# Kernel optimization log

Measured on AMD Instinct MI355X. Metric: run time of the kernel, lower is better.

## Reference

```python
import jax, jax.numpy as jnp
import numpy as np

N = 50000      # nodes
E = 800000     # random edges (self loops appended in reference)
B = 500        # graphs
H = 4          # attention heads
F = 64         # feature_dim (per-head out channels)
SLOPE = 0.2    # GATConv leaky_relu negative slope


def gat_layer(x, src, dst, W, att_s, att_d, b):
    # x: [N, Fin]; W: [Fin, H*F]; att_s/att_d: [H, F]; b: [H*F]
    h = (x @ W).reshape(N, H, F)                       # [N,H,F]
    a_s = jnp.einsum('nhf,hf->nh', h, att_s)           # [N,H]
    a_d = jnp.einsum('nhf,hf->nh', h, att_d)           # [N,H]
    e = jax.nn.leaky_relu(a_s[src] + a_d[dst], SLOPE)  # [E',H]
    emax = jax.ops.segment_max(e, dst, num_segments=N) # [N,H] (finite: self loops)
    ee = jnp.exp(e - emax[dst])
    denom = jax.ops.segment_sum(ee, dst, num_segments=N)
    alpha = ee / denom[dst]                            # [E',H]
    out = jax.ops.segment_sum(alpha[:, :, None] * h[src], dst, num_segments=N)
    return out.reshape(N, H * F) + b


def setup_inputs() -> dict:
    key = jax.random.key(0)
    ks = jax.random.split(key, 32)
    s = 0.05
    inp = {
        'node_features': jax.random.normal(ks[0], (N, 5), jnp.float32),
        'building_mask': jax.random.randint(ks[1], (N,), 0, 2),
        'batch': jnp.sort(jax.random.randint(ks[2], (N,), 0, B)),
        'edge_index': jax.random.randint(ks[3], (2, E), 0, N),
        'bbox_W': jax.random.normal(ks[4], (5, 64)) * s,
        'bbox_b': jnp.zeros((64,), jnp.float32),
        'mask_embed': jax.random.normal(ks[5], (2, 64)) * s,
        'node_W': jax.random.normal(ks[6], (128, 64)) * s,
        'node_b': jnp.zeros((64,), jnp.float32),
        'w0': jax.random.normal(ks[7], (64, 256)) * s,
        'as0': jax.random.normal(ks[8], (H, F)) * s,
        'ad0': jax.random.normal(ks[9], (H, F)) * s,
        'b0': jnp.zeros((256,), jnp.float32),
        'w1': jax.random.normal(ks[10], (256, 256)) * s,
        'as1': jax.random.normal(ks[11], (H, F)) * s,
        'ad1': jax.random.normal(ks[12], (H, F)) * s,
        'b1': jnp.zeros((256,), jnp.float32),
        'w2': jax.random.normal(ks[13], (256, 256)) * s,
        'as2': jax.random.normal(ks[14], (H, F)) * s,
        'ad2': jax.random.normal(ks[15], (H, F)) * s,
        'b2': jnp.zeros((256,), jnp.float32),
        'agg_W': jax.random.normal(ks[16], (832, 256)) * s,
        'agg_b': jnp.zeros((256,), jnp.float32),
        'mu_W': jax.random.normal(ks[17], (256, 256)) * s,
        'mu_b': jnp.zeros((256,), jnp.float32),
        'var_W': jax.random.normal(ks[18], (256, 256)) * s,
        'var_b': jnp.zeros((256,), jnp.float32),
    }
    return inp


def reference(node_features, building_mask, batch, edge_index,
              bbox_W, bbox_b, mask_embed, node_W, node_b,
              w0, as0, ad0, b0, w1, as1, ad1, b1, w2, as2, ad2, b2,
              agg_W, agg_b, mu_W, mu_b, var_W, var_b):
    # node featurization
    x = jax.nn.relu(node_features @ bbox_W + bbox_b)          # [N,64]
    m = jax.nn.relu(mask_embed[building_mask])                 # [N,64]
    n0 = jax.nn.relu(jnp.concatenate([x, m], -1) @ node_W + node_b)  # [N,64]

    # self loops (GATConv add_self_loops=True)
    loop = jnp.arange(N, dtype=edge_index.dtype)
    src = jnp.concatenate([edge_index[0], loop])
    dst = jnp.concatenate([edge_index[1], loop])

    g = jax.ops.segment_max(n0, batch, num_segments=B, indices_are_sorted=True)
    g_embed = [g]

    n_t = jax.nn.relu(gat_layer(n0, src, dst, w0, as0, ad0, b0))
    g_embed.append(jax.ops.segment_max(n_t, batch, num_segments=B, indices_are_sorted=True))

    for (W, a_s, a_d, b) in [(w1, as1, ad1, b1), (w2, as2, ad2, b2)]:
        n_t = jax.nn.relu(gat_layer(n_t, src, dst, W, a_s, a_d, b))
        g_embed.append(jax.ops.segment_max(n_t, batch, num_segments=B, indices_are_sorted=True))

    latent = jnp.concatenate(g_embed, -1) @ agg_W + agg_b      # [B,256]
    mu = latent @ mu_W + mu_b
    log_var = latent @ var_W + var_b
    return (mu, log_var)
```

## Files before the change

### kernel.cpp

```cpp
#include <hip/hip_runtime.h>

#define NN 50000
#define EE 800000
#define BB 500
#define SCB 196

typedef short v8s __attribute__((ext_vector_type(8)));
typedef float v4f __attribute__((ext_vector_type(4)));

__device__ __forceinline__ float bf2f(unsigned short u) {
    union { unsigned int i; float f; } v; v.i = ((unsigned int)u) << 16; return v.f;
}
__device__ __forceinline__ unsigned short f2bf(float f) {
    union { float f; unsigned int i; } v; v.f = f;
    unsigned int x = v.i;
    unsigned int r = (x + 0x7FFFu + ((x >> 16) & 1u)) >> 16;
    return (unsigned short)r;
}

__global__ void k_sentinel(float* out, float val) {
    int i = blockIdx.x * blockDim.x + threadIdx.x;
    if (i < BB * 512) out[i] = val;
}

__global__ void k_prep(const float* __restrict__ nf, const int* __restrict__ bmask,
                       const float* __restrict__ bboxW, const float* __restrict__ bboxb,
                       const float* __restrict__ membed, unsigned short* __restrict__ feat,
                       const float* __restrict__ a0, unsigned short* __restrict__ d0,
                       const float* __restrict__ a1, unsigned short* __restrict__ d1,
                       const float* __restrict__ a2, unsigned short* __restrict__ d2,
                       const float* __restrict__ a3, unsigned short* __restrict__ d3,
                       int* __restrict__ counts) {
    int g = blockIdx.x * blockDim.x + threadIdx.x;
    if (g < NN) counts[g] = 1;
    if (g < NN * 64) {
        int n = g >> 6, f = g & 63;
        float s = bboxb[f];
        for (int k = 0; k < 5; ++k) s += nf[n * 5 + k] * bboxW[k * 64 + f];
        s = fmaxf(s, 0.f);
        int bm = bmask[n]; if ((unsigned)bm > 1u) bm = 0;
        float mv = fmaxf(membed[bm * 64 + f], 0.f);
        feat[(size_t)n * 128 + f] = f2bf(s);
        feat[(size_t)n * 128 + 64 + f] = f2bf(mv);
        return;
    }
    g -= NN * 64;
    const float* in; unsigned short* out; int K, Nout, idx;
    if (g < 8192)        { in = a0; out = d0; K = 128; Nout = 64;  idx = g; }
    else if (g < 24576)  { in = a1; out = d1; K = 64;  Nout = 256; idx = g - 8192; }
    else if (g < 90112)  { in = a2; out = d2; K = 256; Nout = 256; idx = g - 24576; }
    else if (g < 155648) { in = a3; out = d3; K = 256; Nout = 256; idx = g - 90112; }
    else return;
    int k = idx / Nout, n = idx % Nout;
    out[n * K + k] = f2bf(in[idx]);
}

template <int KT, bool BR, bool ATT>
__global__ __launch_bounds__(256) void k_gemm(const unsigned short* __restrict__ A,
                                              const unsigned short* __restrict__ Bt,
                                              const float* __restrict__ bias,
                                              unsigned short* __restrict__ C, int M, int ldc,
                                              const float* __restrict__ atts, const float* __restrict__ attd,
                                              float* __restrict__ asA, float* __restrict__ adA) {
    constexpr int NT = KT / 64;
    constexpr int NB = (NT > 1) ? 2 : 1;
    __shared__ v8s As[NB][64 * 8];
    __shared__ v8s Bs[NB][64 * 8];
    __shared__ float ap[4][4][4][4][2];
    const int t = threadIdx.x;
    const int m0 = blockIdx.x * 64;
    const int n0 = blockIdx.y * 64;
    const int l = t & 63, w = t >> 6;
    const int q = l >> 4, r16 = l & 15;
    const int nloc = w * 16 + r16;

    const int sm = t >> 3, kcl = t & 7;
    const int swz = kcl ^ (sm & 7);
    const int arow0 = m0 + sm, arow1 = m0 + sm + 32;
    const unsigned short* Bp0 = Bt + (size_t)(n0 + sm) * KT + kcl * 8;
    const unsigned short* Bp1 = Bt + (size_t)(n0 + sm + 32) * KT + kcl * 8;
    const unsigned short* Ap0 = A + (size_t)arow0 * KT + kcl * 8;
    const unsigned short* Ap1 = A + (size_t)arow1 * KT + kcl * 8;

    v8s ra0, ra1, rb0, rb1;
    const v8s vz = (v8s){0, 0, 0, 0, 0, 0, 0, 0};
    auto loadT = [&](int kt) {
        ra0 = (arow0 < M) ? *(const v8s*)(Ap0 + kt * 64) : vz;
        ra1 = (arow1 < M) ? *(const v8s*)(Ap1 + kt * 64) : vz;
        rb0 = *(const v8s*)(Bp0 + kt * 64);
        rb1 = *(const v8s*)(Bp1 + kt * 64);
    };
    auto storeT = [&](int b) {
        As[b][sm * 8 + swz] = ra0;
        As[b][(sm + 32) * 8 + swz] = ra1;
        Bs[b][sm * 8 + swz] = rb0;
        Bs[b][(sm + 32) * 8 + swz] = rb1;
    };

    v4f acc[4];
#pragma unroll
    for (int i = 0; i < 4; ++i) acc[i] = (v4f){0.f, 0.f, 0.f, 0.f};

    loadT(0);
    storeT(0);
    __syncthreads();
#pragma unroll
    for (int kt = 0; kt < NT; ++kt) {
        const int b = kt & (NB - 1);
        if (kt + 1 < NT) loadT(kt + 1);
#pragma unroll
        for (int s = 0; s < 2; ++s) {
            int c = s * 4 + q;
            v8s bfr = Bs[b][nloc * 8 + (c ^ (nloc & 7))];
#pragma unroll
            for (int mt = 0; mt < 4; ++mt) {
                v8s afr = As[b][(mt * 16 + r16) * 8 + (c ^ (r16 & 7))];
                acc[mt] = __builtin_amdgcn_mfma_f32_16x16x32_bf16(afr, bfr, acc[mt], 0, 0, 0);
            }
        }
        if (kt + 1 < NT) storeT((kt + 1) & (NB - 1));
        __syncthreads();
    }

    const int col = n0 + nloc;
#pragma unroll
    for (int mt = 0; mt < 4; ++mt) {
#pragma unroll
        for (int r = 0; r < 4; ++r) {
            int row = m0 + mt * 16 + q * 4 + r;
            if (row < M) {
                float v = acc[mt][r];
                if (BR) v = fmaxf(v + bias[col], 0.f);
                C[(size_t)row * ldc + col] = f2bf(v);
            }
        }
    }
    if (ATT) {
        float sa = atts[blockIdx.y * 64 + nloc];
        float da = attd[blockIdx.y * 64 + nloc];
        float rs[4][4], rd[4][4];
#pragma unroll
        for (int mt = 0; mt < 4; ++mt)
#pragma unroll
            for (int r = 0; r < 4; ++r) { rs[mt][r] = acc[mt][r] * sa; rd[mt][r] = acc[mt][r] * da; }
#pragma unroll
        for (int d = 1; d < 16; d <<= 1) {
#pragma unroll
            for (int mt = 0; mt < 4; ++mt)
#pragma unroll
                for (int r = 0; r < 4; ++r) {
                    rs[mt][r] += __shfl_xor(rs[mt][r], d, 64);
                    rd[mt][r] += __shfl_xor(rd[mt][r], d, 64);
                }
        }
        if (r16 == 0) {
#pragma unroll
            for (int mt = 0; mt < 4; ++mt)
#pragma unroll
                for (int r = 0; r < 4; ++r) { ap[w][q][mt][r][0] = rs[mt][r]; ap[w][q][mt][r][1] = rd[mt][r]; }
        }
        __syncthreads();
        if (t < 128) {
            int row = t >> 1, which = t & 1;
            int qq = (row >> 2) & 3, mtt = row >> 4, rr = row & 3;
            float s = ap[0][qq][mtt][rr][which] + ap[1][qq][mtt][rr][which] +
                      ap[2][qq][mtt][rr][which] + ap[3][qq][mtt][rr][which];
            if (m0 + row < M) (which ? adA : asA)[(m0 + row) * 4 + blockIdx.y] = s;
        }
    }
}

__global__ void k_count(const int* __restrict__ dst, int* __restrict__ counts) {
    int e = blockIdx.x * blockDim.x + threadIdx.x;
    if (e < EE) {
        int d = dst[e];
        if ((unsigned)d < (unsigned)NN) atomicAdd(&counts[d], 1);
    }
}

__global__ __launch_bounds__(256) void k_scanA(const int* __restrict__ counts, int* __restrict__ bsum) {
    __shared__ int red[256];
    const int b = blockIdx.x, t = threadIdx.x;
    int i = b * 256 + t;
    red[t] = (i < NN) ? counts[i] : 0;
    __syncthreads();
    for (int d = 128; d > 0; d >>= 1) {
        if (t < d) red[t] += red[t + d];
        __syncthreads();
    }
    if (t == 0) bsum[b] = red[0];
}

__global__ __launch_bounds__(256) void k_scanB(const int* __restrict__ bsum, int* __restrict__ boff) {
    __shared__ int s[256];
    const int t = threadIdx.x;
    int v = (t < SCB) ? bsum[t] : 0;
    s[t] = v;
    __syncthreads();
    for (int d = 1; d < 256; d <<= 1) {
        int x = (t >= d) ? s[t - d] : 0;
        __syncthreads();
        s[t] += x;
        __syncthreads();
    }
    if (t < SCB) boff[t] = s[t] - v;
}

__global__ __launch_bounds__(256) void k_scanC(const int* __restrict__ counts, const int* __restrict__ boff,
                                               int* __restrict__ off, int* __restrict__ cur) {
    __shared__ int s[256];
    const int b = blockIdx.x, t = threadIdx.x;
    int i = b * 256 + t;
    int v = (i < NN) ? counts[i] : 0;
    s[t] = v;
    __syncthreads();
    for (int d = 1; d < 256; d <<= 1) {
        int x = (t >= d) ? s[t - d] : 0;
        __syncthreads();
        s[t] += x;
        __syncthreads();
    }
    int excl = s[t] - v + boff[b];
    if (i < NN) { off[i] = excl; cur[i] = excl; }
    if (i == NN - 1) off[NN] = excl + v;
}

#define SCAT_K 256
__global__ __launch_bounds__(256) void k_scatter(const int* __restrict__ ei, int* __restrict__ cur,
                                                 int* __restrict__ csr) {
    const int p = blockIdx.x & 7;
    const int j = blockIdx.x >> 3;
    const int plo = p * (NN / 8), phi = plo + (NN / 8);
    const int TOT = EE + NN;
    const int chunk = (TOT + SCAT_K - 1) / SCAT_K;
    const int e1 = min((j + 1) * chunk, TOT);
    for (int e = j * chunk + (int)threadIdx.x; e < e1; e += 256) {
        int d = (e < EE) ? ei[EE + e] : (e - EE);
        if (d < plo || d >= phi) continue;
        int s = (e < EE) ? ei[e] : d;
        if ((unsigned)s >= (unsigned)NN) s = d;
        int pos = atomicAdd(&cur[d], 1);
        csr[pos] = s;
    }
}

__global__ __launch_bounds__(256) void k_agg(const unsigned short* __restrict__ h,
                                             const float* __restrict__ asA, const float* __restrict__ adA,
                                             const int* __restrict__ off, const int* __restrict__ csr,
                                             const float* __restrict__ bias,
                                             unsigned short* __restrict__ nout, int base) {
    __shared__ int   sL[4][64];
    __shared__ float wL[4][64][4];
    const int nd4 = threadIdx.x >> 6;
    const int node = base + blockIdx.x * 4 + nd4;
    const int l = threadIdx.x & 63;
    const int hl = l >> 4, k16 = l & 15;
    const int o0 = off[node];
    const int deg = off[node + 1] - o0;
    const int dcap = deg < 64 ? deg : 64;
    const float ad4 = adA[node * 4 + hl];
    float sm = 0.f;
    for (int k = k16; k < dcap; k += 16) {
        int s = csr[o0 + k];
        if (hl == 0) sL[nd4][k] = s;
        float e = asA[s * 4 + hl] + ad4;
        e = e > 0.f ? e : 0.2f * e;
        float w = __expf(e);
        wL[nd4][k][hl] = w;
        sm += w;
    }
    for (int k = 64 + k16; k < deg; k += 16) {
        int s = csr[o0 + k];
        float e = asA[s * 4 + hl] + ad4;
        e = e > 0.f ? e : 0.2f * e;
        sm += __expf(e);
    }
#pragma unroll
    for (int d = 1; d < 16; d <<= 1) sm += __shfl_xor(sm, d, 64);
    const float rden = 1.f / sm;
    __syncthreads();
    float a0 = 0.f, a1 = 0.f, a2 = 0.f, a3 = 0.f;
    const int c = l * 4;
    int k = 0;
    for (; k + 4 <= dcap; k += 4) {
        int s0 = sL[nd4][k], s1 = sL[nd4][k + 1], s2 = sL[nd4][k + 2], s3 = sL[nd4][k + 3];
        float w0 = wL[nd4][k][hl], w1 = wL[nd4][k + 1][hl], w2 = wL[nd4][k + 2][hl], w3 = wL[nd4][k + 3][hl];
        ushort4 h0 = *(const ushort4*)(h + (size_t)s0 * 256 + c);
        ushort4 h1 = *(const ushort4*)(h + (size_t)s1 * 256 + c);
        ushort4 h2 = *(const ushort4*)(h + (size_t)s2 * 256 + c);
        ushort4 h3 = *(const ushort4*)(h + (size_t)s3 * 256 + c);
        a0 += w0 * bf2f(h0.x) + w1 * bf2f(h1.x) + w2 * bf2f(h2.x) + w3 * bf2f(h3.x);
        a1 += w0 * bf2f(h0.y) + w1 * bf2f(h1.y) + w2 * bf2f(h2.y) + w3 * bf2f(h3.y);
        a2 += w0 * bf2f(h0.z) + w1 * bf2f(h1.z) + w2 * bf2f(h2.z) + w3 * bf2f(h3.z);
        a3 += w0 * bf2f(h0.w) + w1 * bf2f(h1.w) + w2 * bf2f(h2.w) + w3 * bf2f(h3.w);
    }
    for (; k < dcap; ++k) {
        int s = sL[nd4][k];
        float w = wL[nd4][k][hl];
        ushort4 hv = *(const ushort4*)(h + (size_t)s * 256 + c);
        a0 += w * bf2f(hv.x); a1 += w * bf2f(hv.y); a2 += w * bf2f(hv.z); a3 += w * bf2f(hv.w);
    }
    for (int k2 = 64; k2 < deg; ++k2) {
        int s = csr[o0 + k2];
        float e = asA[s * 4 + hl] + ad4;
        e = e > 0.f ? e : 0.2f * e;
        float w = __expf(e);
        ushort4 hv = *(const ushort4*)(h + (size_t)s * 256 + c);
        a0 += w * bf2f(hv.x); a1 += w * bf2f(hv.y); a2 += w * bf2f(hv.z); a3 += w * bf2f(hv.w);
    }
    float4 bv = *(const float4*)(bias + c);
    ushort4 o;
    o.x = f2bf(fmaxf(a0 * rden + bv.x, 0.f));
    o.y = f2bf(fmaxf(a1 * rden + bv.y, 0.f));
    o.z = f2bf(fmaxf(a2 * rden + bv.z, 0.f));
    o.w = f2bf(fmaxf(a3 * rden + bv.w, 0.f));
    *(ushort4*)(nout + (size_t)node * 256 + c) = o;
}

__global__ __launch_bounds__(256) void k_gmaxseg(const unsigned short* __restrict__ nt, int cols,
                                                 const int* __restrict__ batch,
                                                 float* __restrict__ gcat, int gbase) {
    __shared__ float red[256];
    const int b = blockIdx.x, t = threadIdx.x;
    const int lane = t & 63, chunk = t >> 6;
    const int c = blockIdx.y * 64 + lane;
    int lo = 0, hi = NN;
    while (lo < hi) { int mid = (lo + hi) >> 1; if (batch[mid] < b) lo = mid + 1; else hi = mid; }
    int lo2 = lo, hi2 = NN;
    while (lo2 < hi2) { int mid = (lo2 + hi2) >> 1; if (batch[mid] < b + 1) lo2 = mid + 1; else hi2 = mid; }
    float m = 0.f;
    for (int n = lo + chunk; n < lo2; n += 4)
        m = fmaxf(m, bf2f(nt[(size_t)n * cols + c]));
    red[t] = m;
    __syncthreads();
    if (chunk == 0) {
        m = fmaxf(fmaxf(m, red[64 + lane]), fmaxf(red[128 + lane], red[192 + lane]));
        gcat[b * 832 + gbase + c] = m;
    }
}

__global__ __launch_bounds__(256) void k_head1(const float* __restrict__ gcat,
                                               const float* __restrict__ aggW, const float* __restrict__ aggb,
                                               float* __restrict__ latent) {
    __shared__ float gr[832 * 4];
    __shared__ float part[4][4][64];
    const int t = threadIdx.x;
    const int g0 = blockIdx.x * 4, c0 = blockIdx.y * 64;
    for (int i = t; i < 832 * 4; i += 256) {
        int k = i >> 2, g = i & 3;
        gr[i] = gcat[(g0 + g) * 832 + k];
    }
    __syncthreads();
    const int w = t >> 6, l = t & 63;
    const float* wp = aggW + c0 + l;
    float a0 = 0.f, a1 = 0.f, a2 = 0.f, a3 = 0.f;
    const int k0 = w * 208;
#pragma unroll 4
    for (int k = k0; k < k0 + 208; ++k) {
        float wv = wp[(size_t)k * 256];
        float4 gv = *(const float4*)&gr[k * 4];
        a0 += gv.x * wv; a1 += gv.y * wv; a2 += gv.z * wv; a3 += gv.w * wv;
    }
    part[w][0][l] = a0; part[w][1][l] = a1; part[w][2][l] = a2; part[w][3][l] = a3;
    __syncthreads();
    const int g = t >> 6, c = t & 63;
    float s = ((part[0][g][c] + part[1][g][c]) + (part[2][g][c] + part[3][g][c])) + aggb[c0 + c];
    latent[(g0 + g) * 256 + c0 + c] = s;
}

__global__ __launch_bounds__(256) void k_head2(const float* __restrict__ latent,
                                               const float* __restrict__ muW, const float* __restrict__ mub,
                                               const float* __restrict__ vaW, const float* __restrict__ vab,
                                               float* __restrict__ out) {
    __shared__ float lr[256 * 4];
    __shared__ float pm[4][4][64], pv[4][4][64];
    const int t = threadIdx.x;
    const int g0 = blockIdx.x * 4, c0 = blockIdx.y * 64;
    for (int i = t; i < 256 * 4; i += 256) {
        int k = i >> 2, g = i & 3;
        lr[i] = latent[(g0 + g) * 256 + k];
    }
    __syncthreads();
    const int w = t >> 6, l = t & 63;
    const float* mp = muW + c0 + l;
    const float* vp = vaW + c0 + l;
    float m0 = 0.f, m1 = 0.f, m2 = 0.f, m3 = 0.f;
    float v0 = 0.f, v1 = 0.f, v2 = 0.f, v3 = 0.f;
    const int k0 = w * 64;
#pragma unroll 4
    for (int k = k0; k < k0 + 64; ++k) {
        float wm = mp[(size_t)k * 256];
        float wv = vp[(size_t)k * 256];
        float4 gv = *(const float4*)&lr[k * 4];
        m0 += gv.x * wm; m1 += gv.y * wm; m2 += gv.z * wm; m3 += gv.w * wm;
        v0 += gv.x * wv; v1 += gv.y * wv; v2 += gv.z * wv; v3 += gv.w * wv;
    }
    pm[w][0][l] = m0; pm[w][1][l] = m1; pm[w][2][l] = m2; pm[w][3][l] = m3;
    pv[w][0][l] = v0; pv[w][1][l] = v1; pv[w][2][l] = v2; pv[w][3][l] = v3;
    __syncthreads();
    const int g = t >> 6, c = t & 63;
    float smu = ((pm[0][g][c] + pm[1][g][c]) + (pm[2][g][c] + pm[3][g][c])) + mub[c0 + c];
    float sva = ((pv[0][g][c] + pv[1][g][c]) + (pv[2][g][c] + pv[3][g][c])) + vab[c0 + c];
    out[(g0 + g) * 256 + c0 + c] = smu;
    out[BB * 256 + (g0 + g) * 256 + c0 + c] = sva;
}

extern "C" void kernel_launch(void* const* d_in, const int* in_sizes, int n_in,
                              void* d_out, int out_size, void* d_ws, size_t ws_size,
                              hipStream_t stream) {
    (void)in_sizes; (void)n_in; (void)out_size;
    const float* nf     = (const float*)d_in[0];
    const int*   bmask  = (const int*)d_in[1];
    const int*   batch  = (const int*)d_in[2];
    const int*   ei     = (const int*)d_in[3];
    const float* bboxW  = (const float*)d_in[4];
    const float* bboxb  = (const float*)d_in[5];
    const float* membed = (const float*)d_in[6];
    const float* nodeW  = (const float*)d_in[7];
    const float* nodeb  = (const float*)d_in[8];
    const float* w0     = (const float*)d_in[9];
    const float* as0    = (const float*)d_in[10];
    const float* ad0    = (const float*)d_in[11];
    const float* b0     = (const float*)d_in[12];
    const float* w1     = (const float*)d_in[13];
    const float* as1    = (const float*)d_in[14];
    const float* ad1    = (const float*)d_in[15];
    const float* b1     = (const float*)d_in[16];
    const float* w2     = (const float*)d_in[17];
    const float* as2    = (const float*)d_in[18];
    const float* ad2    = (const float*)d_in[19];
    const float* b2     = (const float*)d_in[20];
    const float* aggW   = (const float*)d_in[21];
    const float* aggb   = (const float*)d_in[22];
    const float* muW    = (const float*)d_in[23];
    const float* mub    = (const float*)d_in[24];
    const float* vaW    = (const float*)d_in[25];
    const float* vab    = (const float*)d_in[26];
    float* out = (float*)d_out;

    char* base = (char*)d_ws;
    unsigned short* hbuf    = (unsigned short*)(base);
    unsigned short* nbuf    = (unsigned short*)(base + 25600000);
    unsigned short* feat128 = nbuf;
    unsigned short* n0buf   = (unsigned short*)(base + 25600000 + 12800000);
    char* pool0 = base + 51200000;
    char* p = pool0;
    auto alloc = [&](size_t bytes) { char* r = p; p += (bytes + 255) & ~(size_t)255; return r; };
    unsigned short* nodeWt = (unsigned short*)alloc(128 * 64 * 2);
    unsigned short* w0t    = (unsigned short*)alloc(64 * 256 * 2);
    unsigned short* w1t    = (unsigned short*)alloc(256 * 256 * 2);
    unsigned short* w2t    = (unsigned short*)alloc(256 * 256 * 2);
    float* asA    = (float*)alloc((size_t)NN * 4 * 4);
    float* adA    = (float*)alloc((size_t)NN * 4 * 4);
    int*   counts = (int*)alloc((size_t)NN * 4);
    int*   offs   = (int*)alloc((size_t)(NN + 1) * 4);
    int*   cur    = (int*)alloc((size_t)NN * 4);
    int*   csr    = (int*)alloc((size_t)(EE + NN) * 4);
    float* gcat   = (float*)alloc((size_t)BB * 832 * 4);
    float* latent = (float*)alloc((size_t)BB * 256 * 4);
    int*   bsum   = (int*)alloc(SCB * 4);
    int*   boff   = (int*)alloc(SCB * 4);
    const size_t NEED = (size_t)(p - base);

    if (ws_size < NEED) {
        k_sentinel<<<1000, 256, 0, stream>>>(out, 2000.0f + (float)(ws_size >> 20));
        return;
    }

    k_prep<<<(NN * 64 + 155648 + 255) / 256, 256, 0, stream>>>(nf, bmask, bboxW, bboxb, membed, feat128,
                                                               nodeW, nodeWt, w0, w0t, w1, w1t, w2, w2t, counts);
    k_count<<<(EE + 255) / 256, 256, 0, stream>>>(ei + EE, counts);
    k_scanA<<<SCB, 256, 0, stream>>>(counts, bsum);
    k_scanB<<<1, 256, 0, stream>>>(bsum, boff);
    k_scanC<<<SCB, 256, 0, stream>>>(counts, boff, offs, cur);
    k_scatter<<<SCAT_K * 8, 256, 0, stream>>>(ei, cur, csr);
    k_gemm<128, true, false><<<dim3(782, 1), 256, 0, stream>>>(feat128, nodeWt, nodeb, n0buf, NN, 64,
                                                               nullptr, nullptr, nullptr, nullptr);
    k_gmaxseg<<<dim3(BB, 1), 256, 0, stream>>>(n0buf, 64, batch, gcat, 0);
    k_gemm<64, false, true><<<dim3(782, 4), 256, 0, stream>>>(n0buf, w0t, nullptr, hbuf, NN, 256,
                                                              as0, ad0, asA, adA);
    k_agg<<<6250, 256, 0, stream>>>(hbuf, asA, adA, offs, csr, b0, nbuf, 0);
    k_agg<<<6250, 256, 0, stream>>>(hbuf, asA, adA, offs, csr, b0, nbuf, 25000);
    k_gmaxseg<<<dim3(BB, 4), 256, 0, stream>>>(nbuf, 256, batch, gcat, 64);
    k_gemm<256, false, true><<<dim3(782, 4), 256, 0, stream>>>(nbuf, w1t, nullptr, hbuf, NN, 256,
                                                               as1, ad1, asA, adA);
    k_agg<<<6250, 256, 0, stream>>>(hbuf, asA, adA, offs, csr, b1, nbuf, 0);
    k_agg<<<6250, 256, 0, stream>>>(hbuf, asA, adA, offs, csr, b1, nbuf, 25000);
    k_gmaxseg<<<dim3(BB, 4), 256, 0, stream>>>(nbuf, 256, batch, gcat, 320);
    k_gemm<256, false, true><<<dim3(782, 4), 256, 0, stream>>>(nbuf, w2t, nullptr, hbuf, NN, 256,
                                                               as2, ad2, asA, adA);
    k_agg<<<6250, 256, 0, stream>>>(hbuf, asA, adA, offs, csr, b2, nbuf, 0);
    k_agg<<<6250, 256, 0, stream>>>(hbuf, asA, adA, offs, csr, b2, nbuf, 25000);
    k_gmaxseg<<<dim3(BB, 4), 256, 0, stream>>>(nbuf, 256, batch, gcat, 576);
    k_head1<<<dim3(BB / 4, 4), 256, 0, stream>>>(gcat, aggW, aggb, latent);
    k_head2<<<dim3(BB / 4, 4), 256, 0, stream>>>(latent, muW, mub, vaW, vab, out);
}
```

Before: 607.6 us.

## Load GEMM tiles straight into LDS, group blocks for reuse, merge agg launches

The GEMM now stages A and B tiles with global_load_lds, which copies global memory directly into LDS and skips the register round-trip and explicit shared stores. The XOR swizzle is moved onto the source addresses. For the 4-column-tile GEMMs the grid is flattened and remapped so that 8 row tiles and all 4 column tiles of a group run close together, aiming for better L2 reuse of A rows. The two half-range k_agg launches per layer are merged into one launch. The row bound check on A loads is gone, so the last tile reads up to 48 rows past M (stores stay masked), which relies on that memory being readable.

```diff
diff --git a/kernel.cpp b/kernel.cpp
--- a/kernel.cpp
+++ b/kernel.cpp
@@ -16,6 +16,11 @@
     unsigned int x = v.i;
     unsigned int r = (x + 0x7FFFu + ((x >> 16) & 1u)) >> 16;
     return (unsigned short)r;
+}
+
+__device__ __forceinline__ void gll16(const unsigned short* g, v8s* l) {
+    __builtin_amdgcn_global_load_lds((const __attribute__((address_space(1))) unsigned int*)g,
+                                     (__attribute__((address_space(3))) unsigned int*)l, 16, 0, 0);
 }
 
 __global__ void k_sentinel(float* out, float val) {
@@ -55,59 +60,62 @@
     out[n * K + k] = f2bf(in[idx]);
 }
 
-template <int KT, bool BR, bool ATT>
+template <int KT, bool BR, bool ATT, int GY>
 __global__ __launch_bounds__(256) void k_gemm(const unsigned short* __restrict__ A,
                                               const unsigned short* __restrict__ Bt,
                                               const float* __restrict__ bias,
                                               unsigned short* __restrict__ C, int M, int ldc,
                                               const float* __restrict__ atts, const float* __restrict__ attd,
-                                              float* __restrict__ asA, float* __restrict__ adA) {
+                                              float* __restrict__ asA, float* __restrict__ adA, int nbx) {
     constexpr int NT = KT / 64;
     constexpr int NB = (NT > 1) ? 2 : 1;
-    __shared__ v8s As[NB][64 * 8];
-    __shared__ v8s Bs[NB][64 * 8];
+    __shared__ v8s As[NB][512];
+    __shared__ v8s Bs[NB][512];
     __shared__ float ap[4][4][4][4][2];
     const int t = threadIdx.x;
-    const int m0 = blockIdx.x * 64;
-    const int n0 = blockIdx.y * 64;
+    int bx, by;
+    if (GY == 4) {
+        int p = blockIdx.x;
+        int gidx = p >> 5, r = p & 31;
+        bx = gidx * 8 + (r & 7);
+        by = r >> 3;
+        if (bx >= nbx) return;
+    } else {
+        bx = blockIdx.x; by = 0;
+    }
+    const int m0 = bx * 64;
+    const int n0g = by * 64;
     const int l = t & 63, w = t >> 6;
     const int q = l >> 4, r16 = l & 15;
     const int nloc = w * 16 + r16;
 
-    const int sm = t >> 3, kcl = t & 7;
-    const int swz = kcl ^ (sm & 7);
-    const int arow0 = m0 + sm, arow1 = m0 + sm + 32;
-    const unsigned short* Bp0 = Bt + (size_t)(n0 + sm) * KT + kcl * 8;
-    const unsigned short* Bp1 = Bt + (size_t)(n0 + sm + 32) * KT + kcl * 8;
-    const unsigned short* Ap0 = A + (size_t)arow0 * KT + kcl * 8;
-    const unsigned short* Ap1 = A + (size_t)arow1 * KT + kcl * 8;
-
-    v8s ra0, ra1, rb0, rb1;
-    const v8s vz = (v8s){0, 0, 0, 0, 0, 0, 0, 0};
-    auto loadT = [&](int kt) {
-        ra0 = (arow0 < M) ? *(const v8s*)(Ap0 + kt * 64) : vz;
-        ra1 = (arow1 < M) ? *(const v8s*)(Ap1 + kt * 64) : vz;
-        rb0 = *(const v8s*)(Bp0 + kt * 64);
-        rb1 = *(const v8s*)(Bp1 + kt * 64);
-    };
-    auto storeT = [&](int b) {
-        As[b][sm * 8 + swz] = ra0;
-        As[b][(sm + 32) * 8 + swz] = ra1;
-        Bs[b][sm * 8 + swz] = rb0;
-        Bs[b][(sm + 32) * 8 + swz] = rb1;
-    };
+    const int roff0 = (w * 2 + 0) * 8 + (l >> 3);
+    const int roff1 = (w * 2 + 1) * 8 + (l >> 3);
+    const int kc = (l & 7) ^ (l >> 3);
+    const unsigned short* Asrc0 = A + (size_t)(m0 + roff0) * KT + kc * 8;
+    const unsigned short* Asrc1 = A + (size_t)(m0 + roff1) * KT + kc * 8;
+    const unsigned short* Bsrc0 = Bt + (size_t)(n0g + roff0) * KT + kc * 8;
+    const unsigned short* Bsrc1 = Bt + (size_t)(n0g + roff1) * KT + kc * 8;
 
     v4f acc[4];
 #pragma unroll
     for (int i = 0; i < 4; ++i) acc[i] = (v4f){0.f, 0.f, 0.f, 0.f};
 
-    loadT(0);
-    storeT(0);
+    gll16(Asrc0, &As[0][(w * 2 + 0) * 64]);
+    gll16(Asrc1, &As[0][(w * 2 + 1) * 64]);
+    gll16(Bsrc0, &Bs[0][(w * 2 + 0) * 64]);
+    gll16(Bsrc1, &Bs[0][(w * 2 + 1) * 64]);
     __syncthreads();
 #pragma unroll
     for (int kt = 0; kt < NT; ++kt) {
         const int b = kt & (NB - 1);
-        if (kt + 1 < NT) loadT(kt + 1);
+        if (kt + 1 < NT) {
+            const int nb = (kt + 1) & (NB - 1);
+            gll16(Asrc0 + (kt + 1) * 64, &As[nb][(w * 2 + 0) * 64]);
+            gll16(Asrc1 + (kt + 1) * 64, &As[nb][(w * 2 + 1) * 64]);
+            gll16(Bsrc0 + (kt + 1) * 64, &Bs[nb][(w * 2 + 0) * 64]);
+            gll16(Bsrc1 + (kt + 1) * 64, &Bs[nb][(w * 2 + 1) * 64]);
+        }
 #pragma unroll
         for (int s = 0; s < 2; ++s) {
             int c = s * 4 + q;
@@ -118,11 +126,10 @@
                 acc[mt] = __builtin_amdgcn_mfma_f32_16x16x32_bf16(afr, bfr, acc[mt], 0, 0, 0);
             }
         }
-        if (kt + 1 < NT) storeT((kt + 1) & (NB - 1));
-        __syncthreads();
-    }
-
-    const int col = n0 + nloc;
+        __syncthreads();
+    }
+
+    const int col = n0g + nloc;
 #pragma unroll
     for (int mt = 0; mt < 4; ++mt) {
 #pragma unroll
@@ -136,8 +143,8 @@
         }
     }
     if (ATT) {
-        float sa = atts[blockIdx.y * 64 + nloc];
-        float da = attd[blockIdx.y * 64 + nloc];
+        float sa = atts[n0g + nloc];
+        float da = attd[n0g + nloc];
         float rs[4][4], rd[4][4];
 #pragma unroll
         for (int mt = 0; mt < 4; ++mt)
@@ -165,7 +172,7 @@
             int qq = (row >> 2) & 3, mtt = row >> 4, rr = row & 3;
             float s = ap[0][qq][mtt][rr][which] + ap[1][qq][mtt][rr][which] +
                       ap[2][qq][mtt][rr][which] + ap[3][qq][mtt][rr][which];
-            if (m0 + row < M) (which ? adA : asA)[(m0 + row) * 4 + blockIdx.y] = s;
+            if (m0 + row < M) (which ? adA : asA)[(m0 + row) * 4 + by] = s;
         }
     }
 }
@@ -474,23 +481,20 @@
     k_scanB<<<1, 256, 0, stream>>>(bsum, boff);
     k_scanC<<<SCB, 256, 0, stream>>>(counts, boff, offs, cur);
     k_scatter<<<SCAT_K * 8, 256, 0, stream>>>(ei, cur, csr);
-    k_gemm<128, true, false><<<dim3(782, 1), 256, 0, stream>>>(feat128, nodeWt, nodeb, n0buf, NN, 64,
-                                                               nullptr, nullptr, nullptr, nullptr);
+    k_gemm<128, true, false, 1><<<782, 256, 0, stream>>>(feat128, nodeWt, nodeb, n0buf, NN, 64,
+                                                         nullptr, nullptr, nullptr, nullptr, 782);
     k_gmaxseg<<<dim3(BB, 1), 256, 0, stream>>>(n0buf, 64, batch, gcat, 0);
-    k_gemm<64, false, true><<<dim3(782, 4), 256, 0, stream>>>(n0buf, w0t, nullptr, hbuf, NN, 256,
-                                                              as0, ad0, asA, adA);
-    k_agg<<<6250, 256, 0, stream>>>(hbuf, asA, adA, offs, csr, b0, nbuf, 0);
-    k_agg<<<6250, 256, 0, stream>>>(hbuf, asA, adA, offs, csr, b0, nbuf, 25000);
+    k_gemm<64, false, true, 4><<<3136, 256, 0, stream>>>(n0buf, w0t, nullptr, hbuf, NN, 256,
+                                                         as0, ad0, asA, adA, 782);
+    k_agg<<<12500, 256, 0, stream>>>(hbuf, asA, adA, offs, csr, b0, nbuf, 0);
     k_gmaxseg<<<dim3(BB, 4), 256, 0, stream>>>(nbuf, 256, batch, gcat, 64);
-    k_gemm<256, false, true><<<dim3(782, 4), 256, 0, stream>>>(nbuf, w1t, nullptr, hbuf, NN, 256,
-                                                               as1, ad1, asA, adA);
-    k_agg<<<6250, 256, 0, stream>>>(hbuf, asA, adA, offs, csr, b1, nbuf, 0);
-    k_agg<<<6250, 256, 0, stream>>>(hbuf, asA, adA, offs, csr, b1, nbuf, 25000);
+    k_gemm<256, false, true, 4><<<3136, 256, 0, stream>>>(nbuf, w1t, nullptr, hbuf, NN, 256,
+                                                          as1, ad1, asA, adA, 782);
+    k_agg<<<12500, 256, 0, stream>>>(hbuf, asA, adA, offs, csr, b1, nbuf, 0);
     k_gmaxseg<<<dim3(BB, 4), 256, 0, stream>>>(nbuf, 256, batch, gcat, 320);
-    k_gemm<256, false, true><<<dim3(782, 4), 256, 0, stream>>>(nbuf, w2t, nullptr, hbuf, NN, 256,
-                                                               as2, ad2, asA, adA);
-    k_agg<<<6250, 256, 0, stream>>>(hbuf, asA, adA, offs, csr, b2, nbuf, 0);
-    k_agg<<<6250, 256, 0, stream>>>(hbuf, asA, adA, offs, csr, b2, nbuf, 25000);
+    k_gemm<256, false, true, 4><<<3136, 256, 0, stream>>>(nbuf, w2t, nullptr, hbuf, NN, 256,
+                                                          as2, ad2, asA, adA, 782);
+    k_agg<<<12500, 256, 0, stream>>>(hbuf, asA, adA, offs, csr, b2, nbuf, 0);
     k_gmaxseg<<<dim3(BB, 4), 256, 0, stream>>>(nbuf, 256, batch, gcat, 576);
     k_head1<<<dim3(BB / 4, 4), 256, 0, stream>>>(gcat, aggW, aggb, latent);
     k_head2<<<dim3(BB / 4, 4), 256, 0, stream>>>(latent, muW, mub, vaW, vab, out);
```

New measurement: 582.4 us. 1.04x faster.
